# Performance work log

Measured on AMD Instinct MI355X. Metric: run time of the kernel, lower is better.

The kernel has to match this reference:

```python
import jax, jax.numpy as jnp
import numpy as np

S = 1048576   # sequence length (only free scale knob)
D = 20        # d_model (forced == d_internal by the original code)
DI = 20       # d_internal (forced to 20 by output_i[:20])
C = 3         # num_classes
L = 2         # num_layers


def setup_inputs() -> dict:
    key = jax.random.key(0)
    ks = jax.random.split(key, 13)
    f = lambda k, shp, s=1.0: jax.random.normal(k, shp, dtype=jnp.float32) * s
    return {
        "indices": f(ks[0], (S, D)),
        # per-layer stacked parameters (leading axis L)
        "Wq":   f(ks[1], (L, DI, D)),          # torch.randn(d_internal, d)
        "Wk":   f(ks[2], (L, DI, D)),
        "Wv":   f(ks[3], (L, D, D)),           # torch.randn(d, d)
        "Wres": f(ks[4], (L, D, DI)),          # W_residual: (d, d_internal)
        "W1":   f(ks[5], (L, D, DI), 0.2),     # Linear(d_internal, d_model).weight
        "b1":   f(ks[6], (L, D), 0.2),
        "W2":   f(ks[7], (L, D, DI), 0.2),     # second Linear(d_internal, d_model)
        "b2":   f(ks[8], (L, D), 0.2),
        "W3":   f(ks[9], (L, D, D), 0.2),      # Linear(input_dim=d, d_model) residual proj
        "b3":   f(ks[10], (L, D), 0.2),
        "Wc":   f(ks[11], (C, D), 0.2),        # final Linear(d_model, num_classes)
        "bc":   f(ks[12], (C,), 0.2),
    }


def _layer(x, Wq, Wk, Wv, Wres, W1, b1, W2, b2, W3, b3):
    # Vectorized form of the original per-token Python loop.
    q = x @ Wq.T                                   # (S, DI)
    k = x @ Wk.T                                   # (S, DI)
    v = x @ Wv.T                                   # (S, D)
    # scalar similarity per token; softmax over a singleton axis == 1.0 (kept for fidelity)
    sim = jnp.sum(q * k, axis=-1, keepdims=True) / np.sqrt(DI)   # (S, 1)
    p = jax.nn.softmax(sim, axis=-1)               # all ones
    out = (p * v)[:, :DI]                          # output_i = v_i[:20]
    out = out + x @ Wres                           # residual via W_residual
    out = jax.nn.relu(out @ W1.T + b1)             # linear1 + relu
    out = out @ W2.T + b2                          # linear2
    out = out + x @ W3.T + b3                      # final input residual projection
    return out


def reference(indices, Wq, Wk, Wv, Wres, W1, b1, W2, b2, W3, b3, Wc, bc):
    x = indices
    for l in range(L):  # small fixed layer count
        x = _layer(x, Wq[l], Wk[l], Wv[l], Wres[l], W1[l], b1[l], W2[l], b2[l], W3[l], b3[l])
    logits = x @ Wc.T + bc                         # (S, C)
    return jax.nn.softmax(logits, axis=1)
```

## Files before the change

kernel.cpp:

```cpp
#include <hip/hip_runtime.h>
#include <math.h>


#define OFF_G1   0
#define OFF_P1   400
#define OFF_P2   800
#define OFF_M2   1200
#define OFF_Q1   1260
#define OFF_Q2   1320
#define OFF_B11  1380
#define OFF_F2   1400
#define OFF_F3   1420
#define NWTOT    1423

__global__ void prep_kernel(const float* __restrict__ Wv, const float* __restrict__ Wres,
                            const float* __restrict__ W1, const float* __restrict__ b1,
                            const float* __restrict__ W2, const float* __restrict__ b2,
                            const float* __restrict__ W3, const float* __restrict__ b3,
                            const float* __restrict__ Wc, const float* __restrict__ bc,
                            float* __restrict__ W) {
    __shared__ float G2[400];
    __shared__ float M3[60];
    __shared__ float e1[20];
    const int tid = threadIdx.x;
    for (int idx = tid; idx < 480; idx += 256) {
        if (idx < 400) {
            const int i = idx / 20, m = idx % 20;
            float s = 0.f;
            for (int j = 0; j < 20; ++j)
                s = fmaf(Wv[400 + j*20 + i] + Wres[400 + i*20 + j], W1[400 + m*20 + j], s);
            G2[idx] = s;
        } else if (idx < 460) {
            const int r = idx - 400, i = r / 3, c = r % 3;
            float s = 0.f;
            for (int p = 0; p < 20; ++p)
                s = fmaf(Wc[c*20 + p], W3[400 + p*20 + i], s);
            M3[r] = s;
        } else {
            const int j = idx - 460;
            e1[j] = b2[j] + b3[j];
        }
    }
    __syncthreads();
    for (int idx = tid; idx < NWTOT; idx += 256) {
        float s = 0.f;
        if (idx < 400) {
            const int k = idx / 20, m = idx % 20;
            for (int j = 0; j < 20; ++j)
                s = fmaf(Wv[j*20 + k] + Wres[k*20 + j], W1[m*20 + j], s);
        } else if (idx < 800) {
            const int r = idx - 400, mp = r / 20, m = r % 20;
            for (int i = 0; i < 20; ++i)
                s = fmaf(W2[i*20 + mp], G2[i*20 + m], s);
        } else if (idx < 1200) {
            const int r = idx - 800, k = r / 20, m = r % 20;
            for (int i = 0; i < 20; ++i)
                s = fmaf(W3[i*20 + k], G2[i*20 + m], s);
        } else if (idx < 1260) {
            const int r = idx - 1200, c = r / 20, m = r % 20;
            for (int p = 0; p < 20; ++p)
                s = fmaf(Wc[c*20 + p], W2[400 + p*20 + m], s);
        } else if (idx < 1320) {
            const int r = idx - 1260, c = r / 20, mp = r % 20;
            for (int i = 0; i < 20; ++i)
                s = fmaf(W2[i*20 + mp], M3[i*3 + c], s);
        } else if (idx < 1380) {
            const int r = idx - 1320, c = r / 20, k = r % 20;
            for (int i = 0; i < 20; ++i)
                s = fmaf(W3[i*20 + k], M3[i*3 + c], s);
        } else if (idx < 1400) {
            s = b1[idx - 1380];
        } else if (idx < 1420) {
            const int m = idx - 1400;
            s = b1[20 + m];
            for (int i = 0; i < 20; ++i)
                s = fmaf(e1[i], G2[i*20 + m], s);
        } else {
            const int c = idx - 1420;
            s = bc[c];
            for (int p = 0; p < 20; ++p)
                s = fmaf(Wc[c*20 + p], b2[20 + p] + b3[20 + p], s);
            for (int i = 0; i < 20; ++i)
                s = fmaf(e1[i], M3[i*3 + c], s);
        }
        W[idx] = s;
    }
}

__global__ __launch_bounds__(256, 3) void fwd_kernel(const float* __restrict__ X,
                                                     const float* __restrict__ Wg,
                                                     float* __restrict__ out, int npair) {
    __shared__ float Ws[NWTOT + 1];
    for (int i = threadIdx.x; i < NWTOT; i += 256) Ws[i] = Wg[i];
    __syncthreads();

    const int pair = blockIdx.x * blockDim.x + threadIdx.x;
    if (pair >= npair) return;

    const float4* Wv4 = reinterpret_cast<const float4*>(Ws);

    float xa[20], xb[20];
    const float4* xp = reinterpret_cast<const float4*>(X + (size_t)pair * 40);
    #pragma unroll
    for (int q = 0; q < 5; ++q) {
        const float4 v = xp[q];
        xa[4*q+0] = v.x; xa[4*q+1] = v.y; xa[4*q+2] = v.z; xa[4*q+3] = v.w;
    }
    #pragma unroll
    for (int q = 0; q < 5; ++q) {
        const float4 v = xp[5 + q];
        xb[4*q+0] = v.x; xb[4*q+1] = v.y; xb[4*q+2] = v.z; xb[4*q+3] = v.w;
    }

    float ha[20], hb[20];
    #pragma unroll
    for (int q = 0; q < 5; ++q) {
        const float4 b = Wv4[OFF_B11/4 + q];
        ha[4*q+0] = b.x; ha[4*q+1] = b.y; ha[4*q+2] = b.z; ha[4*q+3] = b.w;
        hb[4*q+0] = b.x; hb[4*q+1] = b.y; hb[4*q+2] = b.z; hb[4*q+3] = b.w;
    }
    #pragma unroll
    for (int k = 0; k < 20; ++k) {
        const float x0 = xa[k], x1 = xb[k];
        #pragma unroll
        for (int q = 0; q < 5; ++q) {
            const float4 w = Wv4[OFF_G1/4 + k*5 + q];
            ha[4*q+0] = fmaf(x0, w.x, ha[4*q+0]); hb[4*q+0] = fmaf(x1, w.x, hb[4*q+0]);
            ha[4*q+1] = fmaf(x0, w.y, ha[4*q+1]); hb[4*q+1] = fmaf(x1, w.y, hb[4*q+1]);
            ha[4*q+2] = fmaf(x0, w.z, ha[4*q+2]); hb[4*q+2] = fmaf(x1, w.z, hb[4*q+2]);
            ha[4*q+3] = fmaf(x0, w.w, ha[4*q+3]); hb[4*q+3] = fmaf(x1, w.w, hb[4*q+3]);
        }
    }
    #pragma unroll
    for (int i = 0; i < 20; ++i) { ha[i] = fmaxf(ha[i], 0.f); hb[i] = fmaxf(hb[i], 0.f); }

    float ga[20], gb[20];
    #pragma unroll
    for (int q = 0; q < 5; ++q) {
        const float4 b = Wv4[OFF_F2/4 + q];
        ga[4*q+0] = b.x; ga[4*q+1] = b.y; ga[4*q+2] = b.z; ga[4*q+3] = b.w;
        gb[4*q+0] = b.x; gb[4*q+1] = b.y; gb[4*q+2] = b.z; gb[4*q+3] = b.w;
    }
    #pragma unroll
    for (int k = 0; k < 20; ++k) {
        const float h0 = ha[k], h1 = hb[k];
        #pragma unroll
        for (int q = 0; q < 5; ++q) {
            const float4 w = Wv4[OFF_P1/4 + k*5 + q];
            ga[4*q+0] = fmaf(h0, w.x, ga[4*q+0]); gb[4*q+0] = fmaf(h1, w.x, gb[4*q+0]);
            ga[4*q+1] = fmaf(h0, w.y, ga[4*q+1]); gb[4*q+1] = fmaf(h1, w.y, gb[4*q+1]);
            ga[4*q+2] = fmaf(h0, w.z, ga[4*q+2]); gb[4*q+2] = fmaf(h1, w.z, gb[4*q+2]);
            ga[4*q+3] = fmaf(h0, w.w, ga[4*q+3]); gb[4*q+3] = fmaf(h1, w.w, gb[4*q+3]);
        }
        const float x0 = xa[k], x1 = xb[k];
        #pragma unroll
        for (int q = 0; q < 5; ++q) {
            const float4 w = Wv4[OFF_P2/4 + k*5 + q];
            ga[4*q+0] = fmaf(x0, w.x, ga[4*q+0]); gb[4*q+0] = fmaf(x1, w.x, gb[4*q+0]);
            ga[4*q+1] = fmaf(x0, w.y, ga[4*q+1]); gb[4*q+1] = fmaf(x1, w.y, gb[4*q+1]);
            ga[4*q+2] = fmaf(x0, w.z, ga[4*q+2]); gb[4*q+2] = fmaf(x1, w.z, gb[4*q+2]);
            ga[4*q+3] = fmaf(x0, w.w, ga[4*q+3]); gb[4*q+3] = fmaf(x1, w.w, gb[4*q+3]);
        }
    }
    #pragma unroll
    for (int i = 0; i < 20; ++i) { ga[i] = fmaxf(ga[i], 0.f); gb[i] = fmaxf(gb[i], 0.f); }

    float la[3], lb[3];
    #pragma unroll
    for (int c = 0; c < 3; ++c) {
        float sa = Ws[OFF_F3 + c];
        float sb = sa;
        #pragma unroll
        for (int q = 0; q < 5; ++q) {
            const float4 wm = Wv4[OFF_M2/4 + c*5 + q];
            const float4 wq1 = Wv4[OFF_Q1/4 + c*5 + q];
            const float4 wq2 = Wv4[OFF_Q2/4 + c*5 + q];
            sa = fmaf(ga[4*q+0], wm.x, sa);  sb = fmaf(gb[4*q+0], wm.x, sb);
            sa = fmaf(ga[4*q+1], wm.y, sa);  sb = fmaf(gb[4*q+1], wm.y, sb);
            sa = fmaf(ga[4*q+2], wm.z, sa);  sb = fmaf(gb[4*q+2], wm.z, sb);
            sa = fmaf(ga[4*q+3], wm.w, sa);  sb = fmaf(gb[4*q+3], wm.w, sb);
            sa = fmaf(ha[4*q+0], wq1.x, sa); sb = fmaf(hb[4*q+0], wq1.x, sb);
            sa = fmaf(ha[4*q+1], wq1.y, sa); sb = fmaf(hb[4*q+1], wq1.y, sb);
            sa = fmaf(ha[4*q+2], wq1.z, sa); sb = fmaf(hb[4*q+2], wq1.z, sb);
            sa = fmaf(ha[4*q+3], wq1.w, sa); sb = fmaf(hb[4*q+3], wq1.w, sb);
            sa = fmaf(xa[4*q+0], wq2.x, sa); sb = fmaf(xb[4*q+0], wq2.x, sb);
            sa = fmaf(xa[4*q+1], wq2.y, sa); sb = fmaf(xb[4*q+1], wq2.y, sb);
            sa = fmaf(xa[4*q+2], wq2.z, sa); sb = fmaf(xb[4*q+2], wq2.z, sb);
            sa = fmaf(xa[4*q+3], wq2.w, sa); sb = fmaf(xb[4*q+3], wq2.w, sb);
        }
        la[c] = sa; lb[c] = sb;
    }

    const float ma = fmaxf(fmaxf(la[0], la[1]), la[2]);
    const float ea0 = __expf(la[0] - ma), ea1 = __expf(la[1] - ma), ea2 = __expf(la[2] - ma);
    const float ra = 1.f / (ea0 + ea1 + ea2);
    const float mb = fmaxf(fmaxf(lb[0], lb[1]), lb[2]);
    const float eb0 = __expf(lb[0] - mb), eb1 = __expf(lb[1] - mb), eb2 = __expf(lb[2] - mb);
    const float rb = 1.f / (eb0 + eb1 + eb2);

    float2* o2 = reinterpret_cast<float2*>(out + (size_t)pair * 6);
    o2[0] = make_float2(ea0 * ra, ea1 * ra);
    o2[1] = make_float2(ea2 * ra, eb0 * rb);
    o2[2] = make_float2(eb1 * rb, eb2 * rb);
}

extern "C" void kernel_launch(void* const* d_in, const int* in_sizes, int n_in,
                              void* d_out, int out_size, void* d_ws, size_t ws_size,
                              hipStream_t stream) {
    const float* X    = (const float*)d_in[0];
    const float* Wv   = (const float*)d_in[3];
    const float* Wres = (const float*)d_in[4];
    const float* W1   = (const float*)d_in[5];
    const float* b1   = (const float*)d_in[6];
    const float* W2   = (const float*)d_in[7];
    const float* b2   = (const float*)d_in[8];
    const float* W3   = (const float*)d_in[9];
    const float* b3   = (const float*)d_in[10];
    const float* Wc   = (const float*)d_in[11];
    const float* bc   = (const float*)d_in[12];
    float* out = (float*)d_out;
    float* W   = (float*)d_ws;

    const int S = in_sizes[0] / 20;
    const int npair = S / 2;

    prep_kernel<<<1, 256, 0, stream>>>(Wv, Wres, W1, b1, W2, b2, W3, b3, Wc, bc, W);

    const int block = 256;
    const int grid = (npair + block - 1) / block;
    fwd_kernel<<<grid, block, 0, stream>>>(X, W, out, npair);
}
```

Baseline: 176.3 us.

## Process four tokens per thread and split weight prep into two parallel kernels

The forward kernel now handles four tokens per thread instead of two, so each shared-memory weight load is reused across four rows. The weight-prep stage is split into two kernels so the second stage can use multiple blocks. The logit projections are folded into the main loops through padded float4 tables, and the final ReLU is applied as part of the classifier accumulation. Each thread now holds much more register state, and launch bounds are lowered to two blocks per SM, which reduces occupancy and adds a third kernel launch.

Result: slower. 283.0 us (+60.5%).

```diff
diff --git a/kernel.cpp b/kernel.cpp
--- a/kernel.cpp
+++ b/kernel.cpp
@@ -5,44 +5,50 @@
 #define OFF_G1   0
 #define OFF_P1   400
 #define OFF_P2   800
-#define OFF_M2   1200
-#define OFF_Q1   1260
-#define OFF_Q2   1320
-#define OFF_B11  1380
-#define OFF_F2   1400
-#define OFF_F3   1420
-#define NWTOT    1423
-
-__global__ void prep_kernel(const float* __restrict__ Wv, const float* __restrict__ Wres,
-                            const float* __restrict__ W1, const float* __restrict__ b1,
-                            const float* __restrict__ W2, const float* __restrict__ b2,
-                            const float* __restrict__ W3, const float* __restrict__ b3,
-                            const float* __restrict__ Wc, const float* __restrict__ bc,
-                            float* __restrict__ W) {
-    __shared__ float G2[400];
-    __shared__ float M3[60];
-    __shared__ float e1[20];
-    const int tid = threadIdx.x;
-    for (int idx = tid; idx < 480; idx += 256) {
-        if (idx < 400) {
-            const int i = idx / 20, m = idx % 20;
-            float s = 0.f;
-            for (int j = 0; j < 20; ++j)
-                s = fmaf(Wv[400 + j*20 + i] + Wres[400 + i*20 + j], W1[400 + m*20 + j], s);
-            G2[idx] = s;
-        } else if (idx < 460) {
-            const int r = idx - 400, i = r / 3, c = r % 3;
-            float s = 0.f;
-            for (int p = 0; p < 20; ++p)
-                s = fmaf(Wc[c*20 + p], W3[400 + p*20 + i], s);
-            M3[r] = s;
-        } else {
-            const int j = idx - 460;
-            e1[j] = b2[j] + b3[j];
-        }
-    }
-    __syncthreads();
-    for (int idx = tid; idx < NWTOT; idx += 256) {
+#define OFF_Q1   1200
+#define OFF_Q2   1280
+#define OFF_M2   1360
+#define OFF_B11  1440
+#define OFF_F2   1460
+#define OFF_F3   1480
+#define NW       1484
+#define OFF_G2   1536
+#define OFF_M3   1936
+#define OFF_E1   1996
+
+__global__ void prep1_kernel(const float* __restrict__ Wv, const float* __restrict__ Wres,
+                             const float* __restrict__ W1, const float* __restrict__ b2,
+                             const float* __restrict__ b3, const float* __restrict__ Wc,
+                             const float* __restrict__ W3, float* __restrict__ W) {
+    const int idx = threadIdx.x;
+    if (idx < 400) {
+        const int i = idx / 20, m = idx % 20;
+        float s = 0.f;
+        for (int j = 0; j < 20; ++j)
+            s = fmaf(Wv[400 + j*20 + i] + Wres[400 + i*20 + j], W1[400 + m*20 + j], s);
+        W[OFF_G2 + idx] = s;
+    } else if (idx < 460) {
+        const int r = idx - 400, i = r / 3, c = r % 3;
+        float s = 0.f;
+        for (int p = 0; p < 20; ++p)
+            s = fmaf(Wc[c*20 + p], W3[400 + p*20 + i], s);
+        W[OFF_M3 + r] = s;
+    } else if (idx < 480) {
+        const int j = idx - 460;
+        W[OFF_E1 + j] = b2[j] + b3[j];
+    }
+}
+
+__global__ void prep2_kernel(const float* __restrict__ Wv, const float* __restrict__ Wres,
+                             const float* __restrict__ W1, const float* __restrict__ b1,
+                             const float* __restrict__ W2, const float* __restrict__ b2,
+                             const float* __restrict__ b3, const float* __restrict__ Wc,
+                             const float* __restrict__ bc, const float* __restrict__ W3,
+                             float* __restrict__ W) {
+    const float* G2 = W + OFF_G2;
+    const float* M3 = W + OFF_M3;
+    const float* e1 = W + OFF_E1;
+    for (int idx = blockIdx.x * blockDim.x + threadIdx.x; idx < NW; idx += gridDim.x * blockDim.x) {
         float s = 0.f;
         if (idx < 400) {
             const int k = idx / 20, m = idx % 20;
@@ -56,152 +62,190 @@
             const int r = idx - 800, k = r / 20, m = r % 20;
             for (int i = 0; i < 20; ++i)
                 s = fmaf(W3[i*20 + k], G2[i*20 + m], s);
-        } else if (idx < 1260) {
-            const int r = idx - 1200, c = r / 20, m = r % 20;
-            for (int p = 0; p < 20; ++p)
-                s = fmaf(Wc[c*20 + p], W2[400 + p*20 + m], s);
-        } else if (idx < 1320) {
-            const int r = idx - 1260, c = r / 20, mp = r % 20;
-            for (int i = 0; i < 20; ++i)
-                s = fmaf(W2[i*20 + mp], M3[i*3 + c], s);
-        } else if (idx < 1380) {
-            const int r = idx - 1320, c = r / 20, k = r % 20;
-            for (int i = 0; i < 20; ++i)
-                s = fmaf(W3[i*20 + k], M3[i*3 + c], s);
-        } else if (idx < 1400) {
-            s = b1[idx - 1380];
-        } else if (idx < 1420) {
-            const int m = idx - 1400;
+        } else if (idx < 1280) {
+            const int r = idx - 1200, k = r >> 2, c = r & 3;
+            if (c < 3)
+                for (int i = 0; i < 20; ++i)
+                    s = fmaf(W2[i*20 + k], M3[i*3 + c], s);
+        } else if (idx < 1360) {
+            const int r = idx - 1280, k = r >> 2, c = r & 3;
+            if (c < 3)
+                for (int i = 0; i < 20; ++i)
+                    s = fmaf(W3[i*20 + k], M3[i*3 + c], s);
+        } else if (idx < 1440) {
+            const int r = idx - 1360, m = r >> 2, c = r & 3;
+            if (c < 3)
+                for (int p = 0; p < 20; ++p)
+                    s = fmaf(Wc[c*20 + p], W2[400 + p*20 + m], s);
+        } else if (idx < 1460) {
+            s = b1[idx - 1440];
+        } else if (idx < 1480) {
+            const int m = idx - 1460;
             s = b1[20 + m];
             for (int i = 0; i < 20; ++i)
                 s = fmaf(e1[i], G2[i*20 + m], s);
         } else {
-            const int c = idx - 1420;
-            s = bc[c];
-            for (int p = 0; p < 20; ++p)
-                s = fmaf(Wc[c*20 + p], b2[20 + p] + b3[20 + p], s);
-            for (int i = 0; i < 20; ++i)
-                s = fmaf(e1[i], M3[i*3 + c], s);
+            const int c = idx - 1480;
+            if (c < 3) {
+                s = bc[c];
+                for (int p = 0; p < 20; ++p)
+                    s = fmaf(Wc[c*20 + p], b2[20 + p] + b3[20 + p], s);
+                for (int i = 0; i < 20; ++i)
+                    s = fmaf(e1[i], M3[i*3 + c], s);
+            }
         }
         W[idx] = s;
     }
 }
 
-__global__ __launch_bounds__(256, 3) void fwd_kernel(const float* __restrict__ X,
+__global__ __launch_bounds__(256, 2) void fwd_kernel(const float* __restrict__ X,
                                                      const float* __restrict__ Wg,
-                                                     float* __restrict__ out, int npair) {
-    __shared__ float Ws[NWTOT + 1];
-    for (int i = threadIdx.x; i < NWTOT; i += 256) Ws[i] = Wg[i];
+                                                     float* __restrict__ out, int nquad) {
+    __shared__ float Ws[NW];
+    for (int i = threadIdx.x; i < NW; i += 256) Ws[i] = Wg[i];
     __syncthreads();
 
-    const int pair = blockIdx.x * blockDim.x + threadIdx.x;
-    if (pair >= npair) return;
-
-    const float4* Wv4 = reinterpret_cast<const float4*>(Ws);
-
-    float xa[20], xb[20];
-    const float4* xp = reinterpret_cast<const float4*>(X + (size_t)pair * 40);
-    #pragma unroll
+    const int q4 = blockIdx.x * 256 + threadIdx.x;
+    if (q4 >= nquad) return;
+    const float4* W4 = reinterpret_cast<const float4*>(Ws);
+    const float* xbase = X + (size_t)q4 * 80;
+
+    float h[4][20];
+    #pragma unroll
+    for (int r = 0; r < 5; ++r) {
+        const float4 b = W4[OFF_B11/4 + r];
+        #pragma unroll
+        for (int t = 0; t < 4; ++t) {
+            h[t][4*r+0] = b.x; h[t][4*r+1] = b.y; h[t][4*r+2] = b.z; h[t][4*r+3] = b.w;
+        }
+    }
+    #pragma unroll 1
     for (int q = 0; q < 5; ++q) {
-        const float4 v = xp[q];
-        xa[4*q+0] = v.x; xa[4*q+1] = v.y; xa[4*q+2] = v.z; xa[4*q+3] = v.w;
-    }
-    #pragma unroll
+        float xr[4][4];
+        #pragma unroll
+        for (int t = 0; t < 4; ++t) {
+            const float4 v = *reinterpret_cast<const float4*>(xbase + t*20 + q*4);
+            xr[t][0] = v.x; xr[t][1] = v.y; xr[t][2] = v.z; xr[t][3] = v.w;
+        }
+        #pragma unroll
+        for (int kk = 0; kk < 4; ++kk) {
+            const int k = q*4 + kk;
+            #pragma unroll
+            for (int r = 0; r < 5; ++r) {
+                const float4 w = W4[OFF_G1/4 + k*5 + r];
+                #pragma unroll
+                for (int t = 0; t < 4; ++t) {
+                    h[t][4*r+0] = fmaf(xr[t][kk], w.x, h[t][4*r+0]);
+                    h[t][4*r+1] = fmaf(xr[t][kk], w.y, h[t][4*r+1]);
+                    h[t][4*r+2] = fmaf(xr[t][kk], w.z, h[t][4*r+2]);
+                    h[t][4*r+3] = fmaf(xr[t][kk], w.w, h[t][4*r+3]);
+                }
+            }
+        }
+    }
+    #pragma unroll
+    for (int t = 0; t < 4; ++t)
+        #pragma unroll
+        for (int i = 0; i < 20; ++i) h[t][i] = fmaxf(h[t][i], 0.f);
+
+    float gp[4][20];
+    float l[4][3];
+    #pragma unroll
+    for (int r = 0; r < 5; ++r) {
+        const float4 b = W4[OFF_F2/4 + r];
+        #pragma unroll
+        for (int t = 0; t < 4; ++t) {
+            gp[t][4*r+0] = b.x; gp[t][4*r+1] = b.y; gp[t][4*r+2] = b.z; gp[t][4*r+3] = b.w;
+        }
+    }
+    {
+        const float4 f3 = W4[OFF_F3/4];
+        #pragma unroll
+        for (int t = 0; t < 4; ++t) { l[t][0] = f3.x; l[t][1] = f3.y; l[t][2] = f3.z; }
+    }
+    #pragma unroll 2
+    for (int k = 0; k < 20; ++k) {
+        float hk[4];
+        #pragma unroll
+        for (int t = 0; t < 4; ++t) hk[t] = h[t][k];
+        #pragma unroll
+        for (int r = 0; r < 5; ++r) {
+            const float4 w = W4[OFF_P1/4 + k*5 + r];
+            #pragma unroll
+            for (int t = 0; t < 4; ++t) {
+                gp[t][4*r+0] = fmaf(hk[t], w.x, gp[t][4*r+0]);
+                gp[t][4*r+1] = fmaf(hk[t], w.y, gp[t][4*r+1]);
+                gp[t][4*r+2] = fmaf(hk[t], w.z, gp[t][4*r+2]);
+                gp[t][4*r+3] = fmaf(hk[t], w.w, gp[t][4*r+3]);
+            }
+        }
+        const float4 wq = W4[OFF_Q1/4 + k];
+        #pragma unroll
+        for (int t = 0; t < 4; ++t) {
+            l[t][0] = fmaf(hk[t], wq.x, l[t][0]);
+            l[t][1] = fmaf(hk[t], wq.y, l[t][1]);
+            l[t][2] = fmaf(hk[t], wq.z, l[t][2]);
+        }
+    }
+
+    #pragma unroll 1
     for (int q = 0; q < 5; ++q) {
-        const float4 v = xp[5 + q];
-        xb[4*q+0] = v.x; xb[4*q+1] = v.y; xb[4*q+2] = v.z; xb[4*q+3] = v.w;
-    }
-
-    float ha[20], hb[20];
-    #pragma unroll
-    for (int q = 0; q < 5; ++q) {
-        const float4 b = Wv4[OFF_B11/4 + q];
-        ha[4*q+0] = b.x; ha[4*q+1] = b.y; ha[4*q+2] = b.z; ha[4*q+3] = b.w;
-        hb[4*q+0] = b.x; hb[4*q+1] = b.y; hb[4*q+2] = b.z; hb[4*q+3] = b.w;
-    }
-    #pragma unroll
+        float xr[4][4];
+        #pragma unroll
+        for (int t = 0; t < 4; ++t) {
+            const float4 v = *reinterpret_cast<const float4*>(xbase + t*20 + q*4);
+            xr[t][0] = v.x; xr[t][1] = v.y; xr[t][2] = v.z; xr[t][3] = v.w;
+        }
+        #pragma unroll
+        for (int kk = 0; kk < 4; ++kk) {
+            const int k = q*4 + kk;
+            #pragma unroll
+            for (int r = 0; r < 5; ++r) {
+                const float4 w = W4[OFF_P2/4 + k*5 + r];
+                #pragma unroll
+                for (int t = 0; t < 4; ++t) {
+                    gp[t][4*r+0] = fmaf(xr[t][kk], w.x, gp[t][4*r+0]);
+                    gp[t][4*r+1] = fmaf(xr[t][kk], w.y, gp[t][4*r+1]);
+                    gp[t][4*r+2] = fmaf(xr[t][kk], w.z, gp[t][4*r+2]);
+                    gp[t][4*r+3] = fmaf(xr[t][kk], w.w, gp[t][4*r+3]);
+                }
+            }
+            const float4 wq = W4[OFF_Q2/4 + k];
+            #pragma unroll
+            for (int t = 0; t < 4; ++t) {
+                l[t][0] = fmaf(xr[t][kk], wq.x, l[t][0]);
+                l[t][1] = fmaf(xr[t][kk], wq.y, l[t][1]);
+                l[t][2] = fmaf(xr[t][kk], wq.z, l[t][2]);
+            }
+        }
+    }
+
+    #pragma unroll 4
     for (int k = 0; k < 20; ++k) {
-        const float x0 = xa[k], x1 = xb[k];
-        #pragma unroll
-        for (int q = 0; q < 5; ++q) {
-            const float4 w = Wv4[OFF_G1/4 + k*5 + q];
-            ha[4*q+0] = fmaf(x0, w.x, ha[4*q+0]); hb[4*q+0] = fmaf(x1, w.x, hb[4*q+0]);
-            ha[4*q+1] = fmaf(x0, w.y, ha[4*q+1]); hb[4*q+1] = fmaf(x1, w.y, hb[4*q+1]);
-            ha[4*q+2] = fmaf(x0, w.z, ha[4*q+2]); hb[4*q+2] = fmaf(x1, w.z, hb[4*q+2]);
-            ha[4*q+3] = fmaf(x0, w.w, ha[4*q+3]); hb[4*q+3] = fmaf(x1, w.w, hb[4*q+3]);
-        }
-    }
-    #pragma unroll
-    for (int i = 0; i < 20; ++i) { ha[i] = fmaxf(ha[i], 0.f); hb[i] = fmaxf(hb[i], 0.f); }
-
-    float ga[20], gb[20];
-    #pragma unroll
-    for (int q = 0; q < 5; ++q) {
-        const float4 b = Wv4[OFF_F2/4 + q];
-        ga[4*q+0] = b.x; ga[4*q+1] = b.y; ga[4*q+2] = b.z; ga[4*q+3] = b.w;
-        gb[4*q+0] = b.x; gb[4*q+1] = b.y; gb[4*q+2] = b.z; gb[4*q+3] = b.w;
-    }
-    #pragma unroll
-    for (int k = 0; k < 20; ++k) {
-        const float h0 = ha[k], h1 = hb[k];
-        #pragma unroll
-        for (int q = 0; q < 5; ++q) {
-            const float4 w = Wv4[OFF_P1/4 + k*5 + q];
-            ga[4*q+0] = fmaf(h0, w.x, ga[4*q+0]); gb[4*q+0] = fmaf(h1, w.x, gb[4*q+0]);
-            ga[4*q+1] = fmaf(h0, w.y, ga[4*q+1]); gb[4*q+1] = fmaf(h1, w.y, gb[4*q+1]);
-            ga[4*q+2] = fmaf(h0, w.z, ga[4*q+2]); gb[4*q+2] = fmaf(h1, w.z, gb[4*q+2]);
-            ga[4*q+3] = fmaf(h0, w.w, ga[4*q+3]); gb[4*q+3] = fmaf(h1, w.w, gb[4*q+3]);
-        }
-        const float x0 = xa[k], x1 = xb[k];
-        #pragma unroll
-        for (int q = 0; q < 5; ++q) {
-            const float4 w = Wv4[OFF_P2/4 + k*5 + q];
-            ga[4*q+0] = fmaf(x0, w.x, ga[4*q+0]); gb[4*q+0] = fmaf(x1, w.x, gb[4*q+0]);
-            ga[4*q+1] = fmaf(x0, w.y, ga[4*q+1]); gb[4*q+1] = fmaf(x1, w.y, gb[4*q+1]);
-            ga[4*q+2] = fmaf(x0, w.z, ga[4*q+2]); gb[4*q+2] = fmaf(x1, w.z, gb[4*q+2]);
-            ga[4*q+3] = fmaf(x0, w.w, ga[4*q+3]); gb[4*q+3] = fmaf(x1, w.w, gb[4*q+3]);
-        }
-    }
-    #pragma unroll
-    for (int i = 0; i < 20; ++i) { ga[i] = fmaxf(ga[i], 0.f); gb[i] = fmaxf(gb[i], 0.f); }
-
-    float la[3], lb[3];
-    #pragma unroll
-    for (int c = 0; c < 3; ++c) {
-        float sa = Ws[OFF_F3 + c];
-        float sb = sa;
-        #pragma unroll
-        for (int q = 0; q < 5; ++q) {
-            const float4 wm = Wv4[OFF_M2/4 + c*5 + q];
-            const float4 wq1 = Wv4[OFF_Q1/4 + c*5 + q];
-            const float4 wq2 = Wv4[OFF_Q2/4 + c*5 + q];
-            sa = fmaf(ga[4*q+0], wm.x, sa);  sb = fmaf(gb[4*q+0], wm.x, sb);
-            sa = fmaf(ga[4*q+1], wm.y, sa);  sb = fmaf(gb[4*q+1], wm.y, sb);
-            sa = fmaf(ga[4*q+2], wm.z, sa);  sb = fmaf(gb[4*q+2], wm.z, sb);
-            sa = fmaf(ga[4*q+3], wm.w, sa);  sb = fmaf(gb[4*q+3], wm.w, sb);
-            sa = fmaf(ha[4*q+0], wq1.x, sa); sb = fmaf(hb[4*q+0], wq1.x, sb);
-            sa = fmaf(ha[4*q+1], wq1.y, sa); sb = fmaf(hb[4*q+1], wq1.y, sb);
-            sa = fmaf(ha[4*q+2], wq1.z, sa); sb = fmaf(hb[4*q+2], wq1.z, sb);
-            sa = fmaf(ha[4*q+3], wq1.w, sa); sb = fmaf(hb[4*q+3], wq1.w, sb);
-            sa = fmaf(xa[4*q+0], wq2.x, sa); sb = fmaf(xb[4*q+0], wq2.x, sb);
-            sa = fmaf(xa[4*q+1], wq2.y, sa); sb = fmaf(xb[4*q+1], wq2.y, sb);
-            sa = fmaf(xa[4*q+2], wq2.z, sa); sb = fmaf(xb[4*q+2], wq2.z, sb);
-            sa = fmaf(xa[4*q+3], wq2.w, sa); sb = fmaf(xb[4*q+3], wq2.w, sb);
-        }
-        la[c] = sa; lb[c] = sb;
-    }
-
-    const float ma = fmaxf(fmaxf(la[0], la[1]), la[2]);
-    const float ea0 = __expf(la[0] - ma), ea1 = __expf(la[1] - ma), ea2 = __expf(la[2] - ma);
-    const float ra = 1.f / (ea0 + ea1 + ea2);
-    const float mb = fmaxf(fmaxf(lb[0], lb[1]), lb[2]);
-    const float eb0 = __expf(lb[0] - mb), eb1 = __expf(lb[1] - mb), eb2 = __expf(lb[2] - mb);
-    const float rb = 1.f / (eb0 + eb1 + eb2);
-
-    float2* o2 = reinterpret_cast<float2*>(out + (size_t)pair * 6);
-    o2[0] = make_float2(ea0 * ra, ea1 * ra);
-    o2[1] = make_float2(ea2 * ra, eb0 * rb);
-    o2[2] = make_float2(eb1 * rb, eb2 * rb);
+        const float4 wm = W4[OFF_M2/4 + k];
+        #pragma unroll
+        for (int t = 0; t < 4; ++t) {
+            const float gk = fmaxf(gp[t][k], 0.f);
+            l[t][0] = fmaf(gk, wm.x, l[t][0]);
+            l[t][1] = fmaf(gk, wm.y, l[t][1]);
+            l[t][2] = fmaf(gk, wm.z, l[t][2]);
+        }
+    }
+
+    float o[12];
+    #pragma unroll
+    for (int t = 0; t < 4; ++t) {
+        const float m  = fmaxf(fmaxf(l[t][0], l[t][1]), l[t][2]);
+        const float e0 = __expf(l[t][0] - m);
+        const float e1 = __expf(l[t][1] - m);
+        const float e2 = __expf(l[t][2] - m);
+        const float r  = 1.f / (e0 + e1 + e2);
+        o[3*t+0] = e0 * r; o[3*t+1] = e1 * r; o[3*t+2] = e2 * r;
+    }
+    float4* o4 = reinterpret_cast<float4*>(out + (size_t)q4 * 12);
+    o4[0] = make_float4(o[0], o[1], o[2],  o[3]);
+    o4[1] = make_float4(o[4], o[5], o[6],  o[7]);
+    o4[2] = make_float4(o[8], o[9], o[10], o[11]);
 }
 
 extern "C" void kernel_launch(void* const* d_in, const int* in_sizes, int n_in,
@@ -222,11 +266,12 @@
     float* W   = (float*)d_ws;
 
     const int S = in_sizes[0] / 20;
-    const int npair = S / 2;
-
-    prep_kernel<<<1, 256, 0, stream>>>(Wv, Wres, W1, b1, W2, b2, W3, b3, Wc, bc, W);
+    const int nquad = S / 4;
+
+    prep1_kernel<<<1, 512, 0, stream>>>(Wv, Wres, W1, b2, b3, Wc, W3, W);
+    prep2_kernel<<<4, 256, 0, stream>>>(Wv, Wres, W1, b1, W2, b2, b3, Wc, bc, W3, W);
 
     const int block = 256;
-    const int grid = (npair + block - 1) / block;
-    fwd_kernel<<<grid, block, 0, stream>>>(X, W, out, npair);
-}
+    const int grid = (nquad + block - 1) / block;
+    fwd_kernel<<<grid, block, 0, stream>>>(X, W, out, nquad);
+}
```
